# Kernel tuning notes

Hardware: AMD Instinct MI355X
Metric: run time of the kernel (lower is better)

The kernel has to match this reference:

```python
import jax, jax.numpy as jnp
import numpy as np

B, S, T, E, H, F = 2, 2048, 2048, 1024, 16, 4096
HD = E // H
EPS = 1e-5


def setup_inputs() -> dict:
    key = jax.random.key(0)
    ks = jax.random.split(key, 16)
    def w(k, shape):
        return (jax.random.normal(k, shape, jnp.float32) * 0.02)
    d = {
        "x": jax.random.normal(ks[0], (B, S, E), jnp.float32),
        "enc": jax.random.normal(ks[1], (B, T, E), jnp.float32),
    }
    for i, n in enumerate(["sa_q", "sa_k", "sa_v", "sa_o", "ca_q", "ca_k", "ca_v", "ca_o"]):
        d[n + "w"] = w(ks[2 + i], (E, E))  # torch Linear: [out, in]
        d[n + "b"] = jnp.zeros((E,), jnp.float32)
    d["w1"] = w(ks[10], (F, E)); d["b1"] = jnp.zeros((F,), jnp.float32)
    d["w2"] = w(ks[11], (E, F)); d["b2"] = jnp.zeros((E,), jnp.float32)
    for n in ["ln1", "ln2", "ln3"]:
        d[n + "_g"] = jnp.ones((E,), jnp.float32)
        d[n + "_b"] = jnp.zeros((E,), jnp.float32)
    return d


def _layernorm(x, g, b):
    m = jnp.mean(x, axis=-1, keepdims=True)
    v = jnp.mean((x - m) ** 2, axis=-1, keepdims=True)
    return (x - m) / jnp.sqrt(v + EPS) * g + b


def _heads(x, w, b):
    bsz, sl, _ = x.shape
    y = x @ w.T + b
    return y.reshape(bsz, sl, H, HD).transpose(0, 2, 1, 3)  # [B,H,S,hd]


def _mha(xq, xkv, qw, qb, kw, kb, vw, vb, ow, ob, causal):
    q = _heads(xq, qw, qb)
    k = _heads(xkv, kw, kb)
    v = _heads(xkv, vw, vb)
    scores = jnp.einsum('bhsd,bhtd->bhst', q, k) / np.sqrt(HD).astype(np.float32)
    if causal:
        sl, tl = scores.shape[-2], scores.shape[-1]
        mask = jnp.tril(jnp.ones((sl, tl), bool))
        scores = jnp.where(mask, scores, -jnp.inf)
    a = jax.nn.softmax(scores, axis=-1)
    o = jnp.einsum('bhst,bhtd->bhsd', a, v)
    o = o.transpose(0, 2, 1, 3).reshape(xq.shape[0], xq.shape[1], E)
    return o @ ow.T + ob


def reference(x, enc,
              sa_qw, sa_qb, sa_kw, sa_kb, sa_vw, sa_vb, sa_ow, sa_ob,
              ca_qw, ca_qb, ca_kw, ca_kb, ca_vw, ca_vb, ca_ow, ca_ob,
              w1, b1, w2, b2,
              ln1_g, ln1_b, ln2_g, ln2_b, ln3_g, ln3_b):
    sa = _mha(x, x, sa_qw, sa_qb, sa_kw, sa_kb, sa_vw, sa_vb, sa_ow, sa_ob, True)
    x = _layernorm(x + sa, ln1_g, ln1_b)
    ca = _mha(x, enc, ca_qw, ca_qb, ca_kw, ca_kb, ca_vw, ca_vb, ca_ow, ca_ob, False)
    x = _layernorm(x + ca, ln2_g, ln2_b)
    ffn = jax.nn.relu(x @ w1.T + b1) @ w2.T + b2
    return _layernorm(x + ffn, ln3_g, ln3_b)
```

## Files before the change

kernel.cpp:

```cpp
#include <hip/hip_runtime.h>
#include <hip/hip_bf16.h>
#include <stdint.h>

typedef __attribute__((ext_vector_type(8))) short s16x8;
typedef __attribute__((ext_vector_type(4))) short s16x4;
typedef __attribute__((ext_vector_type(4))) float f32x4;

#define DEV static __device__ __forceinline__

DEV ushort f2bu(float f){
  unsigned u = __builtin_bit_cast(unsigned, f);
  return (ushort)((u + 0x7fffu + ((u >> 16) & 1u)) >> 16);
}
DEV ushort f2bn(float f){
  return __builtin_bit_cast(ushort, __float2bfloat16(f));
}

DEV void gload16(const void* g, void* l){
  __builtin_amdgcn_global_load_lds((const __attribute__((address_space(1))) void*)g,
                                   (__attribute__((address_space(3))) void*)l, 16, 0, 0);
}

#define SCALE_C 0.18033688f

struct ConvArgs {
  const float* src[17];
  void*        dst[17];
  int blk_end[17];
  int nel[17];
  unsigned f32mask;
};

__global__ void __launch_bounds__(256) k_conv(ConvArgs a){
  int bi = blockIdx.x, seg = 0;
  while (bi >= a.blk_end[seg]) seg++;
  int b0 = seg ? a.blk_end[seg-1] : 0;
  long off = (long)(bi - b0)*2048 + (long)threadIdx.x*8;
  if (off >= a.nel[seg]) return;
  const float* s = a.src[seg] + off;
  f32x4 v0 = *(const f32x4*)s;
  f32x4 v1 = *(const f32x4*)(s+4);
  if ((a.f32mask >> seg) & 1u){
    float* d = (float*)a.dst[seg] + off;
    *(f32x4*)d = v0; *(f32x4*)(d+4) = v1;
  } else {
    ushort* d = (ushort*)a.dst[seg] + off;
    s16x8 o;
#pragma unroll
    for (int j = 0; j < 4; j++){ o[j] = (short)f2bu(v0[j]); o[4+j] = (short)f2bu(v1[j]); }
    *(s16x8*)d = o;
  }
}

__global__ void __launch_bounds__(256) k_gemm(const ushort* __restrict__ A, const ushort* __restrict__ W,
    const float* __restrict__ bias, ushort* __restrict__ Cb,
    int M, int N, int K, int lda, int ldb, float scale)
{
  __shared__ __align__(16) ushort lsA[2][128*64];
  __shared__ __align__(16) ushort lsB[2][128*64];
  const int t = threadIdx.x, w = t >> 6, u = t & 63, lr = u & 15, lk = u >> 4;
  const int m0 = blockIdx.y * 128, n0 = blockIdx.x * 128;
  const int wm = w >> 1, wn = w & 1;
  const int rA = t >> 3, c8 = (t & 7) * 8;
  const ushort* Ap = A + (size_t)(m0 + rA) * lda + c8;
  const ushort* Wp = W + (size_t)(n0 + rA) * ldb + c8;
  f32x4 acc[4][4] = {};
  const int nk = K >> 6;

  auto stage = [&](int k0, int buf){
#pragma unroll
    for (int j = 0; j < 4; j++){
      gload16(Ap + (size_t)j*32*lda + k0, &lsA[buf][0] + j*2048 + w*512);
      gload16(Wp + (size_t)j*32*ldb + k0, &lsB[buf][0] + j*2048 + w*512);
    }
  };
  stage(0, 0);
  for (int tk = 0; tk < nk; ++tk){
    __syncthreads();
    if (tk + 1 < nk) stage((tk + 1) << 6, (tk + 1) & 1);
    const ushort* La = &lsA[tk & 1][0];
    const ushort* Lb = &lsB[tk & 1][0];
#pragma unroll
    for (int ks = 0; ks < 2; ks++){
      s16x8 af[4], bfr[4];
#pragma unroll
      for (int i = 0; i < 4; i++) af[i]  = *(const s16x8*)(La + (wm*64 + i*16 + lr)*64 + ks*32 + lk*8);
#pragma unroll
      for (int i = 0; i < 4; i++) bfr[i] = *(const s16x8*)(Lb + (wn*64 + i*16 + lr)*64 + ks*32 + lk*8);
#pragma unroll
      for (int mi = 0; mi < 4; mi++)
#pragma unroll
        for (int ni = 0; ni < 4; ni++)
          acc[mi][ni] = __builtin_amdgcn_mfma_f32_16x16x32_bf16(af[mi], bfr[ni], acc[mi][ni], 0, 0, 0);
    }
  }

#pragma unroll
  for (int mi = 0; mi < 4; mi++){
#pragma unroll
    for (int ni = 0; ni < 4; ni++){
      const int row = m0 + wm*64 + mi*16 + lk*4;
      const int col = n0 + wn*64 + ni*16 + lr;
      const float bv = bias[col];
#pragma unroll
      for (int i = 0; i < 4; i++){
        float v = (acc[mi][ni][i] + bv) * scale;
        Cb[(size_t)(row + i) * N + col] = f2bn(v);
      }
    }
  }
}

__global__ void __launch_bounds__(256) k_gemmS(const ushort* __restrict__ A, const ushort* __restrict__ W,
    const float* __restrict__ bias, float* __restrict__ Cf,
    int M, int N, int Kext, int lda, int ldb, long long sstride)
{
  __shared__ __align__(16) ushort lsA[2][128*64];
  __shared__ __align__(16) ushort lsB[2][128*64];
  const int t = threadIdx.x, w = t >> 6, u = t & 63, lr = u & 15, lk = u >> 4;
  const int m0 = blockIdx.y * 128, n0 = blockIdx.x * 128;
  const int s = blockIdx.z;
  const int wm = w >> 1, wn = w & 1;
  const int rA = t >> 3, c8 = (t & 7) * 8;
  const ushort* Ap = A + (size_t)(m0 + rA) * lda + (size_t)s * Kext + c8;
  const ushort* Wp = W + (size_t)(n0 + rA) * ldb + (size_t)s * Kext + c8;
  if (s){ bias = nullptr; Cf += sstride; }
  f32x4 acc[4][4] = {};
  const int nk = Kext >> 6;

  auto stage = [&](int k0, int buf){
#pragma unroll
    for (int j = 0; j < 4; j++){
      gload16(Ap + (size_t)j*32*lda + k0, &lsA[buf][0] + j*2048 + w*512);
      gload16(Wp + (size_t)j*32*ldb + k0, &lsB[buf][0] + j*2048 + w*512);
    }
  };
  stage(0, 0);
  for (int tk = 0; tk < nk; ++tk){
    __syncthreads();
    if (tk + 1 < nk) stage((tk + 1) << 6, (tk + 1) & 1);
    const ushort* La = &lsA[tk & 1][0];
    const ushort* Lb = &lsB[tk & 1][0];
#pragma unroll
    for (int ks = 0; ks < 2; ks++){
      s16x8 af[4], bfr[4];
#pragma unroll
      for (int i = 0; i < 4; i++) af[i]  = *(const s16x8*)(La + (wm*64 + i*16 + lr)*64 + ks*32 + lk*8);
#pragma unroll
      for (int i = 0; i < 4; i++) bfr[i] = *(const s16x8*)(Lb + (wn*64 + i*16 + lr)*64 + ks*32 + lk*8);
#pragma unroll
      for (int mi = 0; mi < 4; mi++)
#pragma unroll
        for (int ni = 0; ni < 4; ni++)
          acc[mi][ni] = __builtin_amdgcn_mfma_f32_16x16x32_bf16(af[mi], bfr[ni], acc[mi][ni], 0, 0, 0);
    }
  }

#pragma unroll
  for (int mi = 0; mi < 4; mi++){
#pragma unroll
    for (int ni = 0; ni < 4; ni++){
      const int row = m0 + wm*64 + mi*16 + lk*4;
      const int col = n0 + wn*64 + ni*16 + lr;
      const float bv = bias ? bias[col] : 0.f;
#pragma unroll
      for (int i = 0; i < 4; i++)
        Cf[(size_t)(row + i) * N + col] = acc[mi][ni][i] + bv;
    }
  }
}

template<int MODE>
__global__ void __launch_bounds__(512, 1) k_gemm256(const ushort* __restrict__ A, const ushort* __restrict__ W,
    const float* __restrict__ bias, ushort* __restrict__ Cb,
    int N, int Ktot, int lda, int ldb, int scaleLim, float scale)
{
  __shared__ __align__(16) ushort lsA[2][256*64];
  __shared__ __align__(16) ushort lsB[2][256*64];
  const int t = threadIdx.x, w = t >> 6, u = t & 63, lr = u & 15, lk = u >> 4;
  const int gx = gridDim.x;
  const int nwg = gx * gridDim.y;
  const int id = blockIdx.y * gx + blockIdx.x;
  const int swz = (id & 7) * (nwg >> 3) + (id >> 3);
  const int n0 = (swz % gx) * 256, m0 = (swz / gx) * 256;
  const int wm = w >> 2, wn = w & 3;
  const int nt = Ktot >> 6;

  const int r0 = w*8 + (u >> 3), cc = u & 7;
  const int csw = 8 * (cc ^ (r0 & 7));
  const ushort* Ap = A + (size_t)(m0 + r0) * lda + csw;
  const ushort* Wp = W + (size_t)(n0 + r0) * ldb + csw;

  f32x4 acc[8][4] = {};
  const int swl = lr & 7;
  s16x8 afr[4], bfr[4];

#pragma unroll
  for (int j = 0; j < 4; j++){
    gload16(Ap + (size_t)(64*j)*lda, &lsA[0][0] + w*512 + j*4096);
    gload16(Wp + (size_t)(64*j)*ldb, &lsB[0][0] + w*512 + j*4096);
  }
  asm volatile("s_waitcnt vmcnt(0)" ::: "memory");
  __builtin_amdgcn_s_barrier();

  for (int tk = 0; tk < nt; ++tk){
    const char* La = (const char*)&lsA[tk & 1][0];
    const char* Lb = (const char*)&lsB[tk & 1][0];
    ushort* dA = &lsA[(tk & 1) ^ 1][0] + w*512;
    ushort* dB = &lsB[(tk & 1) ^ 1][0] + w*512;
    const bool pf = (tk + 1 < nt);
    const size_t k1 = (size_t)(tk + 1) << 6;

#pragma unroll
    for (int i = 0; i < 4; i++)
      afr[i] = *(const s16x8*)(La + (wm*128 + i*16 + lr)*128 + ((lk ^ swl) * 16));
#pragma unroll
    for (int i = 0; i < 4; i++)
      bfr[i] = *(const s16x8*)(Lb + (wn*64 + i*16 + lr)*128 + ((lk ^ swl) * 16));
    if (pf){
      gload16(Ap + k1, dA);
      gload16(Wp + k1, dB);
      gload16(Ap + (size_t)64*lda + k1, dA + 4096);
      gload16(Wp + (size_t)64*ldb + k1, dB + 4096);
    }
    __builtin_amdgcn_s_barrier();
    asm volatile("s_waitcnt lgkmcnt(0)" ::: "memory");
    __builtin_amdgcn_s_setprio(1);
#pragma unroll
    for (int mi = 0; mi < 4; mi++)
#pragma unroll
      for (int ni = 0; ni < 4; ni++)
        acc[mi][ni] = __builtin_amdgcn_mfma_f32_16x16x32_bf16(afr[mi], bfr[ni], acc[mi][ni], 0, 0, 0);
    __builtin_amdgcn_s_setprio(0);
    __builtin_amdgcn_s_barrier();

#pragma unroll
    for (int i = 0; i < 4; i++)
      afr[i] = *(const s16x8*)(La + (wm*128 + 64 + i*16 + lr)*128 + ((lk ^ swl) * 16));
    if (pf){
      gload16(Ap + (size_t)128*lda + k1, dA + 8192);
      gload16(Wp + (size_t)128*ldb + k1, dB + 8192);
      gload16(Ap + (size_t)192*lda + k1, dA + 12288);
      gload16(Wp + (size_t)192*ldb + k1, dB + 12288);
    }
    __builtin_amdgcn_s_barrier();
    asm volatile("s_waitcnt lgkmcnt(0)" ::: "memory");
    __builtin_amdgcn_s_setprio(1);
#pragma unroll
    for (int mi = 0; mi < 4; mi++)
#pragma unroll
      for (int ni = 0; ni < 4; ni++)
        acc[4+mi][ni] = __builtin_amdgcn_mfma_f32_16x16x32_bf16(afr[mi], bfr[ni], acc[4+mi][ni], 0, 0, 0);
    __builtin_amdgcn_s_setprio(0);
    __builtin_amdgcn_s_barrier();

#pragma unroll
    for (int i = 0; i < 4; i++)
      afr[i] = *(const s16x8*)(La + (wm*128 + i*16 + lr)*128 + (((4 + lk) ^ swl) * 16));
#pragma unroll
    for (int i = 0; i < 4; i++)
      bfr[i] = *(const s16x8*)(Lb + (wn*64 + i*16 + lr)*128 + (((4 + lk) ^ swl) * 16));
    __builtin_amdgcn_s_barrier();
    asm volatile("s_waitcnt lgkmcnt(0)" ::: "memory");
    __builtin_amdgcn_s_setprio(1);
#pragma unroll
    for (int mi = 0; mi < 4; mi++)
#pragma unroll
      for (int ni = 0; ni < 4; ni++)
        acc[mi][ni] = __builtin_amdgcn_mfma_f32_16x16x32_bf16(afr[mi], bfr[ni], acc[mi][ni], 0, 0, 0);
    __builtin_amdgcn_s_setprio(0);
    __builtin_amdgcn_s_barrier();

#pragma unroll
    for (int i = 0; i < 4; i++)
      afr[i] = *(const s16x8*)(La + (wm*128 + 64 + i*16 + lr)*128 + (((4 + lk) ^ swl) * 16));
    __builtin_amdgcn_s_barrier();
    asm volatile("s_waitcnt lgkmcnt(0)" ::: "memory");
    __builtin_amdgcn_s_setprio(1);
#pragma unroll
    for (int mi = 0; mi < 4; mi++)
#pragma unroll
      for (int ni = 0; ni < 4; ni++)
        acc[4+mi][ni] = __builtin_amdgcn_mfma_f32_16x16x32_bf16(afr[mi], bfr[ni], acc[4+mi][ni], 0, 0, 0);
    __builtin_amdgcn_s_setprio(0);
    asm volatile("s_waitcnt vmcnt(0)" ::: "memory");
    __builtin_amdgcn_s_barrier();
  }

#pragma unroll
  for (int mi = 0; mi < 8; mi++){
#pragma unroll
    for (int ni = 0; ni < 4; ni++){
      const int row = m0 + wm*128 + mi*16 + lk*4;
      const int col = n0 + wn*64 + ni*16 + lr;
      const float bv = bias[col];
#pragma unroll
      for (int i = 0; i < 4; i++){
        float v = acc[mi][ni][i] + bv;
        if (MODE == 2) v = fmaxf(v, 0.f);
        if (MODE == 0 && col < scaleLim) v *= scale;
        Cb[(size_t)(row + i) * N + col] = f2bn(v);
      }
    }
  }
}

__global__ void __launch_bounds__(256) k_vt(const ushort* __restrict__ V, ushort* __restrict__ Vt,
                                            int stride, int S)
{
  __shared__ ushort tile[64][72];
  const int st = blockIdx.x*64, h = blockIdx.y, b = blockIdx.z;
  const int r = threadIdx.x >> 3, c8 = (threadIdx.x & 7)*8;
#pragma unroll
  for (int j = 0; j < 2; j++){
    int s = r + j*32;
    s16x8 v = *(const s16x8*)(V + (size_t)(b*S + st + s)*stride + h*64 + c8);
    *(s16x8*)&tile[s][c8] = v;
  }
  __syncthreads();
#pragma unroll
  for (int j = 0; j < 2; j++){
    int d = r + j*32;
    s16x8 o;
#pragma unroll
    for (int e = 0; e < 8; e++) o[e] = tile[c8+e][d];
    *(s16x8*)(Vt + ((size_t)((b*16 + h)*64 + d))*S + st + c8) = o;
  }
}

template<bool CAUSAL>
__global__ void __launch_bounds__(512) k_attn(const ushort* __restrict__ Q, const ushort* __restrict__ Kg,
    const ushort* __restrict__ Vt, ushort* __restrict__ O, int sQ, int sK, int SQ, int SKV)
{
  __shared__ __align__(16) ushort Kl[3][64*64];
  __shared__ __align__(16) ushort Vl[3][64*64];
  __shared__ __align__(16) ushort Pl[8][16*64];
  const int t = threadIdx.x, w = t >> 6, u = t & 63, lr = u & 15, lk = u >> 4;
  const int hb = blockIdx.x;
  const int b = hb >> 4, h = hb & 15;
  const int srow = t >> 3, scol = t & 7;
  const size_t kvbase = (size_t)b * SKV;
  const size_t vtbase = (size_t)((b*16 + h)*64);
  char* Pc = (char*)&Pl[w][0];
  const int swzq = (lr & 7) << 4;

  auto stage = [&](int kt, int buf){
    gload16(Kg + (kvbase + kt*64 + srow)*sK + h*64 + 8*(scol ^ (srow & 7)), &Kl[buf][0] + w*512);
    gload16(Vt + (vtbase + srow)*SKV + kt*64 + 8*(scol ^ (srow & 7)), &Vl[buf][0] + w*512);
  };

  const int NREP = CAUSAL ? 2 : 1;
#pragma unroll 1
  for (int rep = 0; rep < NREP; rep++){
    const int qt = CAUSAL ? (rep ? (int)blockIdx.y : (int)(2*gridDim.y - 1 - blockIdx.y))
                          : (int)blockIdx.y;
    const int q0 = qt * 128;

    const ushort* qp = Q + (size_t)(b*SQ + q0 + w*16 + lr) * sQ + h*64 + lk*8;
    s16x8 qf0 = *(const s16x8*)qp;
    s16x8 qf1 = *(const s16x8*)(qp + 32);

    f32x4 oacc[4] = {};
    f32x4 lacc = {};
    const int nkt = CAUSAL ? (2*qt + 2) : (SKV >> 6);

    asm volatile("s_waitcnt vmcnt(0)" ::: "memory");
    stage(0, 0);
    stage(1, 1);

#pragma unroll 1
    for (int kt = 0; kt < nkt; kt++){
      const int bi = kt % 3;
      const int tn = (kt + 2 < nkt) ? (kt + 2) : (nkt - 1);
      stage(tn, (kt + 2) % 3);
      asm volatile("s_waitcnt vmcnt(4)" ::: "memory");
      __builtin_amdgcn_s_barrier();

      char* Kc = (char*)&Kl[bi][0];
      char* Vc = (char*)&Vl[bi][0];

      f32x4 sacc[4] = {};
      __builtin_amdgcn_s_setprio(1);
#pragma unroll
      for (int ks = 0; ks < 2; ks++){
        s16x8 qf = ks ? qf1 : qf0;
#pragma unroll
        for (int ni = 0; ni < 4; ni++){
          int key = ni*16 + lr;
          s16x8 kf = *(const s16x8*)(Kc + key*128 + ((ks*64 + lk*16) ^ ((key & 7) << 4)));
          sacc[ni] = __builtin_amdgcn_mfma_f32_16x16x32_bf16(kf, qf, sacc[ni], 0, 0, 0);
        }
      }
      __builtin_amdgcn_s_setprio(0);
      if (CAUSAL && kt >= 2*qt){
        const int koff = kt*64 - q0;
#pragma unroll
        for (int ni = 0; ni < 4; ni++)
#pragma unroll
          for (int i = 0; i < 4; i++)
            if (koff + 16*ni + lk*4 + i > w*16 + lr) sacc[ni][i] = -1e30f;
      }

#pragma unroll
      for (int ni = 0; ni < 4; ni++){
#pragma unroll
        for (int i = 0; i < 4; i++) sacc[ni][i] = __builtin_exp2f(sacc[ni][i]);
        lacc += sacc[ni];
      }

#pragma unroll
      for (int ni = 0; ni < 4; ni++){
        s16x4 pk;
#pragma unroll
        for (int i = 0; i < 4; i++) pk[i] = (short)f2bn(sacc[ni][i]);
        *(s16x4*)(Pc + lr*128 + ((32*ni + 8*lk) ^ swzq)) = pk;
      }

      __builtin_amdgcn_s_setprio(1);
#pragma unroll
      for (int ks = 0; ks < 2; ks++){
        s16x8 pf = *(const s16x8*)(Pc + lr*128 + ((ks*64 + lk*16) ^ swzq));
#pragma unroll
        for (int ni = 0; ni < 4; ni++){
          int d = ni*16 + lr;
          s16x8 vf = *(const s16x8*)(Vc + d*128 + ((ks*64 + lk*16) ^ ((d & 7) << 4)));
          oacc[ni] = __builtin_amdgcn_mfma_f32_16x16x32_bf16(pf, vf, oacc[ni], 0, 0, 0);
        }
      }
      __builtin_amdgcn_s_setprio(0);
      __builtin_amdgcn_s_barrier();
    }

    float lrun = lacc[0] + lacc[1] + lacc[2] + lacc[3];
    lrun += __shfl_xor(lrun, 16);
    lrun += __shfl_xor(lrun, 32);
    float il = 1.f / lrun;
    float invl[4];
#pragma unroll
    for (int i = 0; i < 4; i++) invl[i] = __shfl(il, lk*4 + i);
#pragma unroll
    for (int ni = 0; ni < 4; ni++)
#pragma unroll
      for (int i = 0; i < 4; i++)
        O[(size_t)(b*SQ + q0 + w*16 + lk*4 + i)*1024 + h*64 + ni*16 + lr] = f2bn(oacc[ni][i] * invl[i]);
  }
}

template<bool WB16>
__global__ void __launch_bounds__(256) k_ln(const float* __restrict__ R, const float* __restrict__ P,
    const float* __restrict__ P2, const float* __restrict__ G, const float* __restrict__ Bv,
    float* __restrict__ Of, ushort* __restrict__ Ob)
{
  const int row = blockIdx.x, t = threadIdx.x, w = t >> 6, u = t & 63;
  const size_t base = (size_t)row * 1024 + t * 4;
  f32x4 r = *(const f32x4*)(R + base);
  f32x4 p = *(const f32x4*)(P + base);
  f32x4 v = r + p;
  if (P2){ f32x4 p2 = *(const f32x4*)(P2 + base); v += p2; }
  float s = 0.f, q = 0.f;
#pragma unroll
  for (int j = 0; j < 4; j++){ s += v[j]; q += v[j]*v[j]; }
#pragma unroll
  for (int md = 1; md < 64; md <<= 1){ s += __shfl_xor(s, md); q += __shfl_xor(q, md); }
  __shared__ float ps[4], pq[4];
  if (u == 0){ ps[w] = s; pq[w] = q; }
  __syncthreads();
  s = ps[0] + ps[1] + ps[2] + ps[3];
  q = pq[0] + pq[1] + pq[2] + pq[3];
  const float mean = s * (1.f/1024.f);
  const float var  = q * (1.f/1024.f) - mean*mean;
  const float rstd = rsqrtf(var + 1e-5f);
  f32x4 g4 = *(const f32x4*)(G  + t*4);
  f32x4 b4 = *(const f32x4*)(Bv + t*4);
  f32x4 o;
#pragma unroll
  for (int j = 0; j < 4; j++) o[j] = (v[j] - mean) * rstd * g4[j] + b4[j];
  *(f32x4*)(Of + base) = o;
  if (WB16){
    s16x4 ob;
#pragma unroll
    for (int j = 0; j < 4; j++) ob[j] = (short)f2bn(o[j]);
    *(s16x4*)(Ob + base) = ob;
  }
}

extern "C" void kernel_launch(void* const* d_in, const int* in_sizes, int n_in,
                              void* d_out, int out_size, void* d_ws, size_t ws_size,
                              hipStream_t stream)
{
  const float* x   = (const float*)d_in[0];
  const float* enc = (const float*)d_in[1];
  const float* aw[8]; const float* ab[8];
  for (int i = 0; i < 8; i++){ aw[i] = (const float*)d_in[2 + 2*i]; ab[i] = (const float*)d_in[3 + 2*i]; }
  const float* w1 = (const float*)d_in[18]; const float* b1 = (const float*)d_in[19];
  const float* w2 = (const float*)d_in[20]; const float* b2 = (const float*)d_in[21];
  const float* lg[3] = {(const float*)d_in[22], (const float*)d_in[24], (const float*)d_in[26]};
  const float* lb[3] = {(const float*)d_in[23], (const float*)d_in[25], (const float*)d_in[27]};
  float* out = (float*)d_out;

  const size_t MB = 1024ull * 1024ull;
  if (ws_size < 129 * MB) return;
  char* ws = (char*)d_ws;
  ushort* wqkv = (ushort*)(ws + 0*MB);
  ushort* wcq  = (ushort*)(ws + 6*MB);
  ushort* wkv  = (ushort*)(ws + 8*MB);
  ushort* wo1w = (ushort*)(ws + 12*MB);
  ushort* wo2w = (ushort*)(ws + 14*MB);
  ushort* w1b  = (ushort*)(ws + 16*MB);
  ushort* w2b  = (ushort*)(ws + 24*MB);
  ushort* xb   = (ushort*)(ws + 32*MB);
  ushort* encb = (ushort*)(ws + 40*MB);
  ushort* attb = (ushort*)(ws + 48*MB);
  float*  proj = (float*)(ws + 56*MB);
  float*  x1f  = (float*)(ws + 72*MB);
  ushort* xab  = (ushort*)(ws + 88*MB);
  ushort* QKVb    = (ushort*)(ws + 96*MB);
  ushort* Vt1     = (ushort*)(ws + 120*MB);
  ushort* crossQb = (ushort*)(ws + 96*MB);
  ushort* encKVb  = (ushort*)(ws + 104*MB);
  ushort* Vt2     = (ushort*)(ws + 120*MB);
  ushort* hb      = (ushort*)(ws + 96*MB);
  float*  pWO     = (float*)(ws + 96*MB);
  float*  pFF     = (float*)(ws + 32*MB);
  float*  bqkv = (float*)(ws + 128*MB);
  float*  bkv  = (float*)(ws + 128*MB + 16384);

  const long long ssWO  = ((long long)(96 - 56) * (long long)MB) / 4;
  const long long ssFFN = ((long long)(32 - 56) * (long long)MB) / 4;

  ConvArgs ca;
  const float* srcs[17] = { x, enc, aw[0], aw[1], aw[2], aw[3], aw[4], aw[5], aw[6], aw[7],
                            w1, w2, ab[0], ab[1], ab[2], ab[5], ab[6] };
  void* dsts[17] = { xb, encb, wqkv, wqkv + 1048576, wqkv + 2097152, wo1w, wcq, wkv, wkv + 1048576, wo2w,
                     w1b, w2b, bqkv, bqkv + 1024, bqkv + 2048, bkv, bkv + 1024 };
  int nels[17] = { 4194304, 4194304, 1048576, 1048576, 1048576, 1048576, 1048576, 1048576, 1048576, 1048576,
                   4194304, 4194304, 1024, 1024, 1024, 1024, 1024 };
  int acc_blk = 0;
  for (int i = 0; i < 17; i++){
    ca.src[i] = srcs[i]; ca.dst[i] = dsts[i]; ca.nel[i] = nels[i];
    acc_blk += (nels[i] + 2047) / 2048;
    ca.blk_end[i] = acc_blk;
  }
  ca.f32mask = 0x1F000u;
  k_conv<<<acc_blk, 256, 0, stream>>>(ca);

  k_gemm256<0><<<dim3(12,16), 512, 0, stream>>>(xb, wqkv, bqkv, QKVb, 3072, 1024, 1024, 1024, 1024, SCALE_C);
  k_vt<<<dim3(32,16,2), 256, 0, stream>>>(QKVb + 2048, Vt1, 3072, 2048);
  k_attn<true><<<dim3(32,8), 512, 0, stream>>>(QKVb, QKVb + 1024, Vt1, attb, 3072, 3072, 2048, 2048);
  k_gemmS<<<dim3(8,32,2), 256, 0, stream>>>(attb, wo1w, ab[3], proj, 4096, 1024, 512, 1024, 1024, ssWO);
  k_ln<true><<<4096, 256, 0, stream>>>(x, proj, pWO, lg[0], lb[0], x1f, xab);

  k_gemm<<<dim3(8,32), 256, 0, stream>>>(xab, wcq, ab[4], crossQb, 4096, 1024, 1024, 1024, 1024, SCALE_C);
  k_gemm256<0><<<dim3(8,16), 512, 0, stream>>>(encb, wkv, bkv, encKVb, 2048, 1024, 1024, 1024, 0, 1.f);
  k_vt<<<dim3(32,16,2), 256, 0, stream>>>(encKVb + 1024, Vt2, 2048, 2048);
  k_attn<false><<<dim3(32,16), 512, 0, stream>>>(crossQb, encKVb, Vt2, attb, 1024, 2048, 2048, 2048);
  k_gemmS<<<dim3(8,32,2), 256, 0, stream>>>(attb, wo2w, ab[7], proj, 4096, 1024, 512, 1024, 1024, ssWO);
  k_ln<true><<<4096, 256, 0, stream>>>(x1f, proj, pWO, lg[1], lb[1], x1f, xab);

  k_gemm256<2><<<dim3(16,16), 512, 0, stream>>>(xab, w1b, b1, hb, 4096, 1024, 1024, 1024, 0, 1.f);
  k_gemmS<<<dim3(8,32,2), 256, 0, stream>>>(hb, w2b, b2, proj, 4096, 1024, 2048, 4096, 4096, ssFFN);
  k_ln<false><<<4096, 256, 0, stream>>>(x1f, proj, pFF, lg[2], lb[2], out, nullptr);
}
```

Before: 399.8 us.

## Merge cross-attn Q and encoder KV GEMMs; double-buffer attention with MFMA row sums

The cross-attention Q projection and the encoder K/V projection now run as one grouped GEMM launch, with block ids split between the two problems. This removes a kernel launch and lets the two small GEMMs fill the GPU together. The attention kernel moves from triple-buffered K/V staging with explicit waitcnt and barrier to double buffering with __syncthreads, which cuts shared memory use but overlaps loads less deeply. The softmax denominator is now taken from an extra MFMA against a ones vector on the bf16 P tile, replacing the per-lane sums and shuffle reduction.

```diff
diff --git a/kernel.cpp b/kernel.cpp
--- a/kernel.cpp
+++ b/kernel.cpp
@@ -2,9 +2,9 @@
 #include <hip/hip_bf16.h>
 #include <stdint.h>
 
-typedef __attribute__((ext_vector_type(8))) short s16x8;
-typedef __attribute__((ext_vector_type(4))) short s16x4;
-typedef __attribute__((ext_vector_type(4))) float f32x4;
+typedef __attribute__((ext_vector_type(8)))  short s16x8;
+typedef __attribute__((ext_vector_type(4)))  short s16x4;
+typedef __attribute__((ext_vector_type(4)))  float f32x4;
 
 #define DEV static __device__ __forceinline__
 
@@ -52,32 +52,35 @@
   }
 }
 
-__global__ void __launch_bounds__(256) k_gemm(const ushort* __restrict__ A, const ushort* __restrict__ W,
-    const float* __restrict__ bias, ushort* __restrict__ Cb,
-    int M, int N, int K, int lda, int ldb, float scale)
+__global__ void __launch_bounds__(256) k_gemmB(const ushort* __restrict__ A0, const ushort* __restrict__ W0,
+    const float* __restrict__ b0, ushort* __restrict__ C0,
+    const ushort* __restrict__ A1, const ushort* __restrict__ W1,
+    const float* __restrict__ b1, ushort* __restrict__ C1, float scale0)
 {
   __shared__ __align__(16) ushort lsA[2][128*64];
   __shared__ __align__(16) ushort lsB[2][128*64];
   const int t = threadIdx.x, w = t >> 6, u = t & 63, lr = u & 15, lk = u >> 4;
-  const int m0 = blockIdx.y * 128, n0 = blockIdx.x * 128;
+  const int bid = blockIdx.x;
+  const ushort *A, *W; const float* bias; ushort* C; int N, n0, m0; float scale;
+  if (bid < 256){ A = A0; W = W0; bias = b0; C = C0; N = 1024; n0 = (bid & 7)*128;  m0 = (bid >> 3)*128; scale = scale0; }
+  else { int i2 = bid - 256; A = A1; W = W1; bias = b1; C = C1; N = 2048; n0 = (i2 & 15)*128; m0 = (i2 >> 4)*128; scale = 1.f; }
   const int wm = w >> 1, wn = w & 1;
   const int rA = t >> 3, c8 = (t & 7) * 8;
-  const ushort* Ap = A + (size_t)(m0 + rA) * lda + c8;
-  const ushort* Wp = W + (size_t)(n0 + rA) * ldb + c8;
+  const ushort* Ap = A + (size_t)(m0 + rA) * 1024 + c8;
+  const ushort* Wp = W + (size_t)(n0 + rA) * 1024 + c8;
   f32x4 acc[4][4] = {};
-  const int nk = K >> 6;
 
   auto stage = [&](int k0, int buf){
 #pragma unroll
     for (int j = 0; j < 4; j++){
-      gload16(Ap + (size_t)j*32*lda + k0, &lsA[buf][0] + j*2048 + w*512);
-      gload16(Wp + (size_t)j*32*ldb + k0, &lsB[buf][0] + j*2048 + w*512);
+      gload16(Ap + (size_t)j*32*1024 + k0, &lsA[buf][0] + j*2048 + w*512);
+      gload16(Wp + (size_t)j*32*1024 + k0, &lsB[buf][0] + j*2048 + w*512);
     }
   };
   stage(0, 0);
-  for (int tk = 0; tk < nk; ++tk){
+  for (int tk = 0; tk < 16; ++tk){
     __syncthreads();
-    if (tk + 1 < nk) stage((tk + 1) << 6, (tk + 1) & 1);
+    if (tk + 1 < 16) stage((tk + 1) << 6, (tk + 1) & 1);
     const ushort* La = &lsA[tk & 1][0];
     const ushort* Lb = &lsB[tk & 1][0];
 #pragma unroll
@@ -105,7 +108,7 @@
 #pragma unroll
       for (int i = 0; i < 4; i++){
         float v = (acc[mi][ni][i] + bv) * scale;
-        Cb[(size_t)(row + i) * N + col] = f2bn(v);
+        C[(size_t)(row + i) * N + col] = f2bn(v);
       }
     }
   }
@@ -332,8 +335,8 @@
 __global__ void __launch_bounds__(512) k_attn(const ushort* __restrict__ Q, const ushort* __restrict__ Kg,
     const ushort* __restrict__ Vt, ushort* __restrict__ O, int sQ, int sK, int SQ, int SKV)
 {
-  __shared__ __align__(16) ushort Kl[3][64*64];
-  __shared__ __align__(16) ushort Vl[3][64*64];
+  __shared__ __align__(16) ushort Kl[2][64*64];
+  __shared__ __align__(16) ushort Vl[2][64*64];
   __shared__ __align__(16) ushort Pl[8][16*64];
   const int t = threadIdx.x, w = t >> 6, u = t & 63, lr = u & 15, lk = u >> 4;
   const int hb = blockIdx.x;
@@ -344,6 +347,10 @@
   char* Pc = (char*)&Pl[w][0];
   const int swzq = (lr & 7) << 4;
 
+  s16x8 ONES;
+#pragma unroll
+  for (int j = 0; j < 8; j++) ONES[j] = (short)0x3F80;
+
   auto stage = [&](int kt, int buf){
     gload16(Kg + (kvbase + kt*64 + srow)*sK + h*64 + 8*(scol ^ (srow & 7)), &Kl[buf][0] + w*512);
     gload16(Vt + (vtbase + srow)*SKV + kt*64 + 8*(scol ^ (srow & 7)), &Vl[buf][0] + w*512);
@@ -361,23 +368,17 @@
     s16x8 qf1 = *(const s16x8*)(qp + 32);
 
     f32x4 oacc[4] = {};
-    f32x4 lacc = {};
+    f32x4 lsum = {};
     const int nkt = CAUSAL ? (2*qt + 2) : (SKV >> 6);
 
-    asm volatile("s_waitcnt vmcnt(0)" ::: "memory");
     stage(0, 0);
-    stage(1, 1);
-
-#pragma unroll 1
+    __syncthreads();
+
     for (int kt = 0; kt < nkt; kt++){
-      const int bi = kt % 3;
-      const int tn = (kt + 2 < nkt) ? (kt + 2) : (nkt - 1);
-      stage(tn, (kt + 2) % 3);
-      asm volatile("s_waitcnt vmcnt(4)" ::: "memory");
-      __builtin_amdgcn_s_barrier();
-
-      char* Kc = (char*)&Kl[bi][0];
-      char* Vc = (char*)&Vl[bi][0];
+      const int buf = kt & 1;
+      if (kt + 1 < nkt) stage(kt + 1, buf ^ 1);
+      char* Kc = (char*)&Kl[buf][0];
+      char* Vc = (char*)&Vl[buf][0];
 
       f32x4 sacc[4] = {};
       __builtin_amdgcn_s_setprio(1);
@@ -402,11 +403,9 @@
       }
 
 #pragma unroll
-      for (int ni = 0; ni < 4; ni++){
+      for (int ni = 0; ni < 4; ni++)
 #pragma unroll
         for (int i = 0; i < 4; i++) sacc[ni][i] = __builtin_exp2f(sacc[ni][i]);
-        lacc += sacc[ni];
-      }
 
 #pragma unroll
       for (int ni = 0; ni < 4; ni++){
@@ -420,6 +419,7 @@
 #pragma unroll
       for (int ks = 0; ks < 2; ks++){
         s16x8 pf = *(const s16x8*)(Pc + lr*128 + ((ks*64 + lk*16) ^ swzq));
+        lsum = __builtin_amdgcn_mfma_f32_16x16x32_bf16(pf, ONES, lsum, 0, 0, 0);
 #pragma unroll
         for (int ni = 0; ni < 4; ni++){
           int d = ni*16 + lr;
@@ -428,16 +428,12 @@
         }
       }
       __builtin_amdgcn_s_setprio(0);
-      __builtin_amdgcn_s_barrier();
-    }
-
-    float lrun = lacc[0] + lacc[1] + lacc[2] + lacc[3];
-    lrun += __shfl_xor(lrun, 16);
-    lrun += __shfl_xor(lrun, 32);
-    float il = 1.f / lrun;
+      __syncthreads();
+    }
+
     float invl[4];
 #pragma unroll
-    for (int i = 0; i < 4; i++) invl[i] = __shfl(il, lk*4 + i);
+    for (int i = 0; i < 4; i++) invl[i] = 1.f / lsum[i];
 #pragma unroll
     for (int ni = 0; ni < 4; ni++)
 #pragma unroll
@@ -550,8 +546,7 @@
   k_gemmS<<<dim3(8,32,2), 256, 0, stream>>>(attb, wo1w, ab[3], proj, 4096, 1024, 512, 1024, 1024, ssWO);
   k_ln<true><<<4096, 256, 0, stream>>>(x, proj, pWO, lg[0], lb[0], x1f, xab);
 
-  k_gemm<<<dim3(8,32), 256, 0, stream>>>(xab, wcq, ab[4], crossQb, 4096, 1024, 1024, 1024, 1024, SCALE_C);
-  k_gemm256<0><<<dim3(8,16), 512, 0, stream>>>(encb, wkv, bkv, encKVb, 2048, 1024, 1024, 1024, 0, 1.f);
+  k_gemmB<<<768, 256, 0, stream>>>(xab, wcq, ab[4], crossQb, encb, wkv, bkv, encKVb, SCALE_C);
   k_vt<<<dim3(32,16,2), 256, 0, stream>>>(encKVb + 1024, Vt2, 2048, 2048);
   k_attn<false><<<dim3(32,16), 512, 0, stream>>>(crossQb, encKVb, Vt2, attb, 1024, 2048, 2048, 2048);
   k_gemmS<<<dim3(8,32,2), 256, 0, stream>>>(attb, wo2w, ab[7], proj, 4096, 1024, 512, 1024, 1024, ssWO);
```

Result: no change. 398.6 us (-0.3%).
